# Performance work log

Measured on AMD Instinct MI355X. Metric: run time of the kernel, lower is better.

Reference implementation:

```python
import jax, jax.numpy as jnp
import numpy as np

N = 50000   # nodes
E = 800000  # edges
G = 256     # graphs in batch
NF, EF, H, L = 16, 8, 128, 4
EPS = 1e-5


def setup_inputs() -> dict:
    key = jax.random.key(0)
    ks = jax.random.split(key, 20)
    s = 0.05
    return {
        "x": jax.random.normal(ks[0], (N, NF), jnp.float32),
        "edge_index": jax.random.randint(ks[1], (2, E), 0, N, dtype=jnp.int32),
        "edge_attr": jax.random.uniform(ks[2], (E, EF), jnp.float32),
        "batch": jnp.sort(jax.random.randint(ks[3], (N,), 0, G, dtype=jnp.int32)),
        "W_emb": jax.random.normal(ks[4], (NF, H), jnp.float32) * s,
        "b_emb": jnp.zeros((H,), jnp.float32),
        "Wf": jax.random.normal(ks[5], (L, 2 * H + EF, H), jnp.float32) * s,
        "bf": jnp.zeros((L, H), jnp.float32),
        "Ws": jax.random.normal(ks[6], (L, 2 * H + EF, H), jnp.float32) * s,
        "bs": jnp.zeros((L, H), jnp.float32),
        "gamma": jnp.ones((L, H), jnp.float32),
        "beta": jnp.zeros((L, H), jnp.float32),
        "W1": jax.random.normal(ks[7], (H, 64), jnp.float32) * s,
        "b1": jnp.zeros((64,), jnp.float32),
        "W2": jax.random.normal(ks[8], (64, 32), jnp.float32) * s,
        "b2": jnp.zeros((32,), jnp.float32),
        "W_out": jax.random.normal(ks[9], (32, 1), jnp.float32) * s,
        "b_out": jnp.zeros((1,), jnp.float32),
    }


def reference(x, edge_index, edge_attr, batch, W_emb, b_emb, Wf, bf, Ws, bs,
              gamma, beta, W1, b1, W2, b2, W_out, b_out):
    src, dst = edge_index[0], edge_index[1]  # message j->i: x_j=h[src], x_i=h[dst]
    h = jax.nn.relu(x @ W_emb + b_emb)       # [N, H]
    for l in range(L):
        # CGConv: z_ij = [x_i, x_j, e_ij]; gated message; sum-aggregate; +x residual
        z = jnp.concatenate([h[dst], h[src], edge_attr], axis=-1)  # [E, 2H+EF]
        m = jax.nn.sigmoid(z @ Wf[l] + bf[l]) * jax.nn.softplus(z @ Ws[l] + bs[l])
        agg = jax.ops.segment_sum(m, dst, num_segments=N)
        x_new = agg + h
        # BatchNorm1d (training-mode batch statistics, biased var)
        mu = x_new.mean(axis=0)
        var = x_new.var(axis=0)
        x_new = gamma[l] * (x_new - mu) * jax.lax.rsqrt(var + EPS) + beta[l]
        x_new = jax.nn.relu(x_new)
        h = h + x_new
    # global mean pool over graphs
    cnt = jax.ops.segment_sum(jnp.ones((N,), h.dtype), batch, num_segments=G)
    pooled = jax.ops.segment_sum(h, batch, num_segments=G) / jnp.maximum(cnt, 1.0)[:, None]
    g = jax.nn.relu(pooled @ W1 + b1)
    g = jax.nn.relu(g @ W2 + b2)
    return (g @ W_out + b_out).squeeze(-1)  # [G]
```

## Files before the change

kernel.cpp:

```cpp
#include <hip/hip_runtime.h>
#include <hip/hip_bf16.h>

#define H 128
#define EFD 8
#define NLAYER 4
#define ZDIM (2*H+EFD)

typedef float f32x2 __attribute__((ext_vector_type(2)));
typedef float f32x4 __attribute__((ext_vector_type(4)));
typedef short s16x8 __attribute__((ext_vector_type(8)));
typedef _Float16 f16x4 __attribute__((ext_vector_type(4)));

#define PKFMA_LO(acc, a, b) asm("v_pk_fma_f32 %0, %1, %2, %0 op_sel:[0,0,0] op_sel_hi:[0,1,1]" : "+v"(acc) : "v"(a), "v"(b))
#define PKFMA_HI(acc, a, b) asm("v_pk_fma_f32 %0, %1, %2, %0 op_sel:[1,0,0] op_sel_hi:[1,1,1]" : "+v"(acc) : "v"(a), "v"(b))
#define PKFMA_LO_INIT(dst, a, b, c) asm("v_pk_fma_f32 %0, %1, %2, %3 op_sel:[0,0,0] op_sel_hi:[0,1,1]" : "=v"(dst) : "v"(a), "v"(b), "v"(c))

#define L2E 1.44269504088896340736f
#define LN2 0.69314718055994530942f

__device__ __forceinline__ unsigned short f2bf(float x){
    unsigned u = __float_as_uint(x);
    return (unsigned short)((u + 0x7FFFu + ((u>>16)&1u)) >> 16);
}

__global__ void embed_kernel(const float* __restrict__ x, const float* __restrict__ We,
                             const float* __restrict__ be, float* __restrict__ h, int N){
    int idx = blockIdx.x*blockDim.x + threadIdx.x;
    if (idx >= N*H) return;
    int n = idx >> 7, f = idx & 127;
    float a = be[f];
    #pragma unroll
    for (int k=0;k<16;k++) a = fmaf(x[n*16+k], We[k*H+f], a);
    h[idx] = fmaxf(a, 0.f);
}

__global__ void hist_kernel(const int* __restrict__ dstI, int* __restrict__ counts, int E){
    int e = blockIdx.x*blockDim.x + threadIdx.x;
    if (e < E) atomicAdd(&counts[dstI[e]], 1);
}

__global__ __launch_bounds__(1024) void scan1(const int* __restrict__ counts, int* __restrict__ incl,
                                              int* __restrict__ bsums, int N){
    __shared__ int lds[1024];
    int t = threadIdx.x;
    int i = blockIdx.x*1024 + t;
    int v = (i < N) ? counts[i] : 0;
    lds[t] = v;
    __syncthreads();
    for (int off=1; off<1024; off<<=1){
        int add = (t>=off) ? lds[t-off] : 0;
        __syncthreads();
        lds[t] += add;
        __syncthreads();
    }
    if (i < N) incl[i] = lds[t];
    if (t == 1023) bsums[blockIdx.x] = lds[1023];
}

__global__ void scan2(int* bsums, int nb){
    if (threadIdx.x == 0){
        int run = 0;
        for (int b=0;b<nb;b++){ int v = bsums[b]; bsums[b] = run; run += v; }
    }
}

__global__ __launch_bounds__(1024) void scan3(const int* incl, const int* __restrict__ counts,
                                              const int* __restrict__ bsums, int* __restrict__ rowptr,
                                              int* cursor, int N, int E){
    int i = blockIdx.x*1024 + threadIdx.x;
    if (i >= N) return;
    int ex = incl[i] - counts[i] + bsums[blockIdx.x];
    rowptr[i] = ex;
    cursor[i] = ex;
    if (i == N-1) rowptr[N] = E;
}

__global__ void scatter_kernel(const int* __restrict__ srcI, const int* __restrict__ dstI,
                               const float* __restrict__ eattr, int* __restrict__ cursor,
                               int* __restrict__ src_s, float* __restrict__ ea_s, int E){
    int e = blockIdx.x*blockDim.x + threadIdx.x;
    if (e >= E) return;
    int d = dstI[e];
    int pos = atomicAdd(&cursor[d], 1);
    src_s[pos] = srcI[e];
    const float4* s4 = (const float4*)(eattr + (size_t)e*EFD);
    float4* o4 = (float4*)(ea_s + (size_t)pos*EFD);
    o4[0] = s4[0]; o4[1] = s4[1];
}

__global__ __launch_bounds__(256) void wpack_kernel(const float* __restrict__ Wf, const float* __restrict__ Ws,
        s16x8* __restrict__ bhi, s16x8* __restrict__ blo){
    int idx = blockIdx.x*256 + threadIdx.x;
    int l = idx & 63, ct = (idx>>6)&7, ks = (idx>>9)&3, w = (idx>>11)&3, layer = idx>>13;
    int cp = w*128 + ct*16 + (l&15);
    int k0 = ks*32 + ((l>>4)<<3);
    const float* WfL = Wf + (size_t)layer*ZDIM*H;
    const float* WsL = Ws + (size_t)layer*ZDIM*H;
    int colIn = cp & 127;
    int sel = cp >> 7;
    const float* Wm = (sel & 1) ? WsL : WfL;
    int krow = (sel >> 1) ? H : 0;
    s16x8 vh, vl;
    #pragma unroll
    for (int e=0;e<8;e++){
        float v = Wm[(size_t)(krow + k0 + e)*H + colIn];
        unsigned short hb = f2bf(v);
        float rem = v - __uint_as_float(((unsigned)hb)<<16);
        vh[e] = (short)hb;
        vl[e] = (short)f2bf(rem);
    }
    bhi[idx] = vh;
    blo[idx] = vl;
}

__global__ __launch_bounds__(512, 2) void table_mfma(
        float* __restrict__ h, const float* __restrict__ xn, const float* __restrict__ scsh,
        const s16x8* __restrict__ bhi, const s16x8* __restrict__ blo,
        const float* __restrict__ bf_l, const float* __restrict__ bs_l,
        float* __restrict__ TD, _Float16* __restrict__ TS16, int N, int layer, int ntiles){
    __shared__ __align__(16) short amat[2][32*136];
    const int t = threadIdx.x;
    const int lane = t & 63, W = t >> 6;
    const int ow = W >> 1, ctbase = (W & 1)*4;
    const int rbase = lane & 15, kg = lane >> 4;

    s16x8 Bh[4][4], Bl[4][4];
    {
        const size_t bbase = ((size_t)layer*4 + ow)*2048;
        #pragma unroll
        for (int ks=0;ks<4;ks++)
            #pragma unroll
            for (int c=0;c<4;c++){
                Bh[ks][c] = bhi[bbase + ks*512 + (ctbase+c)*64 + lane];
                Bl[ks][c] = blo[bbase + ks*512 + (ctbase+c)*64 + lane];
            }
        #pragma unroll
        for (int ks=0;ks<4;ks++)
            #pragma unroll
            for (int c=0;c<4;c++) asm volatile("" : "+v"(Bh[ks][c]), "+v"(Bl[ks][c]));
    }
    int c_local[4], off16[4];
    float bv[4];
    #pragma unroll
    for (int c=0;c<4;c++){
        c_local[c] = (ctbase+c)*16 + rbase;
        off16[c] = (c_local[c] >> 1)*4 + ((ow & 1) << 1) + (c_local[c] & 1);
        bv[c] = (ow == 0) ? bf_l[c_local[c]]*L2E : (ow == 1) ? bs_l[c_local[c]]*L2E : 0.f;
    }
    const int srow = t >> 4;
    const int kb = (t & 15)*8;
    float sc8[8], sh8[8];
    if (scsh){
        #pragma unroll
        for (int q=0;q<8;q+=4){
            *(float4*)&sc8[q] = *(const float4*)(scsh + kb + q);
            *(float4*)&sh8[q] = *(const float4*)(scsh + H + kb + q);
        }
    }

    for (int tile = blockIdx.x; tile < ntiles; tile += gridDim.x){
        const int n0 = tile*32;
        {
            const int gn = n0 + srow;
            const bool valid = gn < N;
            float* hr = h + (size_t)gn*H + kb;
            float vv[8];
            if (scsh){
                const float* xr = xn + (size_t)gn*H + kb;
                #pragma unroll
                for (int q=0;q<8;q+=4){
                    float4 xv = valid ? *(const float4*)(xr + q) : make_float4(0.f,0.f,0.f,0.f);
                    float4 hv = valid ? *(const float4*)(hr + q) : make_float4(0.f,0.f,0.f,0.f);
                    vv[q]   = hv.x + fmaxf(fmaf(xv.x, sc8[q],   sh8[q]),   0.f);
                    vv[q+1] = hv.y + fmaxf(fmaf(xv.y, sc8[q+1], sh8[q+1]), 0.f);
                    vv[q+2] = hv.z + fmaxf(fmaf(xv.z, sc8[q+2], sh8[q+2]), 0.f);
                    vv[q+3] = hv.w + fmaxf(fmaf(xv.w, sc8[q+3], sh8[q+3]), 0.f);
                }
                if (valid){
                    #pragma unroll
                    for (int q=0;q<8;q+=4){
                        float4 o; o.x=vv[q]; o.y=vv[q+1]; o.z=vv[q+2]; o.w=vv[q+3];
                        *(float4*)(hr + q) = o;
                    }
                }
            } else {
                #pragma unroll
                for (int q=0;q<8;q+=4){
                    float4 hv = valid ? *(const float4*)(hr + q) : make_float4(0.f,0.f,0.f,0.f);
                    vv[q]=hv.x; vv[q+1]=hv.y; vv[q+2]=hv.z; vv[q+3]=hv.w;
                }
            }
            s16x8 hv2, lv2;
            #pragma unroll
            for (int q=0;q<8;q++){
                unsigned short hb = f2bf(vv[q]);
                float rem = vv[q] - __uint_as_float(((unsigned)hb)<<16);
                hv2[q] = (short)hb;
                lv2[q] = (short)f2bf(rem);
            }
            *(s16x8*)&amat[0][srow*136 + kb] = hv2;
            *(s16x8*)&amat[1][srow*136 + kb] = lv2;
        }
        __syncthreads();
        f32x4 acc[2][4];
        #pragma unroll
        for (int rt=0;rt<2;rt++)
            #pragma unroll
            for (int c=0;c<4;c++){ acc[rt][c][0]=0.f; acc[rt][c][1]=0.f; acc[rt][c][2]=0.f; acc[rt][c][3]=0.f; }
        #pragma unroll
        for (int ks=0;ks<4;ks++){
            s16x8 ah[2], al[2];
            #pragma unroll
            for (int rt=0;rt<2;rt++){
                const int ao = (rbase + 16*rt)*136 + ks*32 + kg*8;
                ah[rt] = *(const s16x8*)&amat[0][ao];
                al[rt] = *(const s16x8*)&amat[1][ao];
            }
            #pragma unroll
            for (int c=0;c<4;c++)
                #pragma unroll
                for (int rt=0;rt<2;rt++){
                    acc[rt][c] = __builtin_amdgcn_mfma_f32_16x16x32_bf16(ah[rt], Bh[ks][c], acc[rt][c], 0, 0, 0);
                    acc[rt][c] = __builtin_amdgcn_mfma_f32_16x16x32_bf16(ah[rt], Bl[ks][c], acc[rt][c], 0, 0, 0);
                    acc[rt][c] = __builtin_amdgcn_mfma_f32_16x16x32_bf16(al[rt], Bh[ks][c], acc[rt][c], 0, 0, 0);
                }
        }
        if (ow < 2){
            const int colbase = (ow & 1)*128;
            #pragma unroll
            for (int c=0;c<4;c++)
                #pragma unroll
                for (int rt=0;rt<2;rt++){
                    const int nrow0 = n0 + 16*rt + kg*4;
                    #pragma unroll
                    for (int r=0;r<4;r++){
                        const int nd = nrow0 + r;
                        if (nd < N) TD[(size_t)nd*256 + colbase + c_local[c]] = fmaf(acc[rt][c][r], L2E, bv[c]);
                    }
                }
        } else {
            #pragma unroll
            for (int c=0;c<4;c++)
                #pragma unroll
                for (int rt=0;rt<2;rt++){
                    const int nrow0 = n0 + 16*rt + kg*4;
                    #pragma unroll
                    for (int r=0;r<4;r++){
                        const int nd = nrow0 + r;
                        if (nd < N) TS16[(size_t)nd*256 + off16[c]] = (_Float16)(acc[rt][c][r]*L2E);
                    }
                }
        }
        __syncthreads();
    }
}

__global__ __launch_bounds__(256, 4) void agg_kernel(
        const float* __restrict__ TD, const _Float16* __restrict__ TS16,
        const int* __restrict__ rowptr, const int* __restrict__ src_s, const float* __restrict__ ea_s,
        const float* __restrict__ Wf_l, const float* __restrict__ Ws_l,
        const float* __restrict__ h, float* __restrict__ xn, int N){
    __shared__ float wE[2048];
    const int t = threadIdx.x;
    {
        const float4* a = (const float4*)(Wf_l + 2*H*H);
        const float4* b = (const float4*)(Ws_l + 2*H*H);
        float4 va = a[t], vb = b[t];
        va.x*=L2E; va.y*=L2E; va.z*=L2E; va.w*=L2E;
        vb.x*=L2E; vb.y*=L2E; vb.z*=L2E; vb.w*=L2E;
        ((float4*)wE)[t] = va;
        ((float4*)wE)[256 + t] = vb;
    }
    __syncthreads();
    const int k = t & 63;
    const int i = blockIdx.x*4 + (t >> 6);
    if (i >= N) return;
    f32x2 wef2[8], wes2[8];
    #pragma unroll
    for (int r=0;r<8;r++){
        wef2[r] = *(const f32x2*)&wE[r*128 + 2*k];
        wes2[r] = *(const f32x2*)&wE[1024 + r*128 + 2*k];
    }
    #pragma unroll
    for (int r=0;r<8;r++) asm volatile("" : "+v"(wef2[r]), "+v"(wes2[r]));
    const f32x2* td = (const f32x2*)(TD + ((size_t)i << 8));
    f32x2 fd2 = td[k], sd2 = td[64+k];
    f32x2 acc = {0.f, 0.f};
    const int e0 = __builtin_amdgcn_readfirstlane(rowptr[i]);
    const int e1 = __builtin_amdgcn_readfirstlane(rowptr[i+1]);
    const int myoff = 4*k;
    int j = (e0 < e1) ? __builtin_amdgcn_readfirstlane(src_s[e0]) : 0;
    f16x4 tv = *(const f16x4*)(TS16 + (((size_t)(unsigned)j) << 8) + myoff);
    for (int e = e0; e < e1; ++e){
        const int en = (e+1 < e1) ? (e+1) : e;
        const int jn = __builtin_amdgcn_readfirstlane(src_s[en]);
        f16x4 tvn = *(const f16x4*)(TS16 + (((size_t)(unsigned)jn) << 8) + myoff);
        const float* ep = ea_s + (size_t)e*EFD;
        f32x4 eaA = *(const f32x4*)(ep);
        f32x4 eaB = *(const f32x4*)(ep + 4);
        f32x2 ea0 = __builtin_shufflevector(eaA, eaA, 0, 1);
        f32x2 ea1 = __builtin_shufflevector(eaA, eaA, 2, 3);
        f32x2 ea2 = __builtin_shufflevector(eaB, eaB, 0, 1);
        f32x2 ea3 = __builtin_shufflevector(eaB, eaB, 2, 3);
        f32x2 ef, es;
        PKFMA_LO_INIT(ef, ea0, wef2[0], fd2);
        PKFMA_HI(ef, ea0, wef2[1]);
        PKFMA_LO(ef, ea1, wef2[2]); PKFMA_HI(ef, ea1, wef2[3]);
        PKFMA_LO(ef, ea2, wef2[4]); PKFMA_HI(ef, ea2, wef2[5]);
        PKFMA_LO(ef, ea3, wef2[6]); PKFMA_HI(ef, ea3, wef2[7]);
        PKFMA_LO_INIT(es, ea0, wes2[0], sd2);
        PKFMA_HI(es, ea0, wes2[1]);
        PKFMA_LO(es, ea1, wes2[2]); PKFMA_HI(es, ea1, wes2[3]);
        PKFMA_LO(es, ea2, wes2[4]); PKFMA_HI(es, ea2, wes2[5]);
        PKFMA_LO(es, ea3, wes2[6]); PKFMA_HI(es, ea3, wes2[7]);
        f32x2 g = ef, p = es;
        g.x += (float)tv[0]; g.y += (float)tv[1];
        p.x += (float)tv[2]; p.y += (float)tv[3];
        float sx = __builtin_amdgcn_rcpf(1.0f + __builtin_amdgcn_exp2f(-g.x));
        float sy = __builtin_amdgcn_rcpf(1.0f + __builtin_amdgcn_exp2f(-g.y));
        float tx = fmaxf(p.x, 0.f) + __builtin_amdgcn_logf(1.0f + __builtin_amdgcn_exp2f(-fabsf(p.x)));
        float ty = fmaxf(p.y, 0.f) + __builtin_amdgcn_logf(1.0f + __builtin_amdgcn_exp2f(-fabsf(p.y)));
        acc.x = fmaf(sx*tx, LN2, acc.x);
        acc.y = fmaf(sy*ty, LN2, acc.y);
        tv = tvn; j = jn;
    }
    f32x2 hv = *(const f32x2*)(h + ((size_t)i << 7) + 2*k);
    f32x2 o = acc + hv;
    *(f32x2*)(xn + ((size_t)i << 7) + 2*k) = o;
}

__global__ __launch_bounds__(256) void stats_kernel(const float* __restrict__ xn, double* __restrict__ sums, int N){
    __shared__ double l1[128], l2[128];
    const int f = threadIdx.x & 127;
    const int half = threadIdx.x >> 7;
    const int nb = gridDim.x;
    const int per = (N + nb - 1)/nb;
    const int r0 = blockIdx.x*per;
    const int r1 = min(N, r0+per);
    double s = 0.0, s2 = 0.0;
    for (int r=r0+half; r<r1; r+=2){
        float v = xn[(size_t)r*H + f];
        s += v; s2 += (double)v*(double)v;
    }
    if (half == 1){ l1[f] = s; l2[f] = s2; }
    __syncthreads();
    if (half == 0){
        s += l1[f]; s2 += l2[f];
        atomicAdd(&sums[f], s);
        atomicAdd(&sums[H+f], s2);
    }
}

__global__ void finalize_bn(double* __restrict__ sums, const float* __restrict__ gamma_l,
                            const float* __restrict__ beta_l, float* __restrict__ scsh, int N){
    int f = threadIdx.x;
    if (f >= H) return;
    double mu = sums[f]/(double)N;
    double var = sums[H+f]/(double)N - mu*mu;
    if (var < 0.0) var = 0.0;
    float sc = (float)((double)gamma_l[f] / sqrt(var + 1e-5));
    scsh[f]   = sc;
    scsh[H+f] = (float)((double)beta_l[f] - mu*(double)sc);
    sums[f] = 0.0;
    sums[H+f] = 0.0;
}

__global__ __launch_bounds__(128) void pool_mlp_kernel(const float* __restrict__ h, const float* __restrict__ xn,
        const float* __restrict__ scsh, const int* __restrict__ batch,
        const float* __restrict__ W1, const float* __restrict__ b1,
        const float* __restrict__ W2, const float* __restrict__ b2,
        const float* __restrict__ Wo, const float* __restrict__ bo,
        float* __restrict__ out, int N){
    __shared__ float row[128];
    __shared__ float g1[64];
    __shared__ float g2[32];
    const int g = blockIdx.x;
    const int t = threadIdx.x;
    int lo = 0, hi = N;
    while (lo < hi){ int m = (lo+hi)>>1; if (batch[m] < g) lo = m+1; else hi = m; }
    const int s0 = lo;
    hi = N;
    while (lo < hi){ int m = (lo+hi)>>1; if (batch[m] < g+1) lo = m+1; else hi = m; }
    const int s1 = lo;
    const float sc = scsh[t], sh = scsh[H+t];
    float acc = 0.f;
    for (int r = s0; r < s1; ++r){
        float hv = h[(size_t)r*H + t];
        float xv = xn[(size_t)r*H + t];
        acc += hv + fmaxf(fmaf(xv, sc, sh), 0.f);
    }
    const float inv = 1.0f/fmaxf((float)(s1-s0), 1.0f);
    row[t] = acc*inv;
    __syncthreads();
    if (t < 64){
        float a = b1[t];
        #pragma unroll 4
        for (int i2=0;i2<128;i2++) a = fmaf(row[i2], W1[i2*64+t], a);
        g1[t] = fmaxf(a, 0.f);
    }
    __syncthreads();
    if (t < 32){
        float b = b2[t];
        #pragma unroll 4
        for (int i2=0;i2<64;i2++) b = fmaf(g1[i2], W2[i2*32+t], b);
        g2[t] = fmaxf(b, 0.f);
    }
    __syncthreads();
    if (t < 64){
        float p = (t < 32) ? g2[t]*Wo[t] : 0.f;
        for (int off=32; off>0; off>>=1) p += __shfl_down(p, off);
        if (t == 0) out[g] = p + bo[0];
    }
}

extern "C" void kernel_launch(void* const* d_in, const int* in_sizes, int n_in,
                              void* d_out, int out_size, void* d_ws, size_t ws_size,
                              hipStream_t stream){
    const float* x     = (const float*)d_in[0];
    const int*   eidx  = (const int*)d_in[1];
    const float* eattr = (const float*)d_in[2];
    const int*   batch = (const int*)d_in[3];
    const float* W_emb = (const float*)d_in[4];
    const float* b_emb = (const float*)d_in[5];
    const float* Wf    = (const float*)d_in[6];
    const float* bf    = (const float*)d_in[7];
    const float* Wsm   = (const float*)d_in[8];
    const float* bs    = (const float*)d_in[9];
    const float* gamma = (const float*)d_in[10];
    const float* beta  = (const float*)d_in[11];
    const float* W1    = (const float*)d_in[12];
    const float* b1    = (const float*)d_in[13];
    const float* W2    = (const float*)d_in[14];
    const float* b2    = (const float*)d_in[15];
    const float* Wo    = (const float*)d_in[16];
    const float* bo    = (const float*)d_in[17];
    float* out = (float*)d_out;

    const int N = in_sizes[0]/16;
    const int E = in_sizes[1]/2;
    const int G = out_size;

    const int* srcI = eidx;
    const int* dstI = eidx + E;

    char* p = (char*)d_ws;
    auto alloc = [&](size_t bytes)->char*{ char* r = p; p += (bytes + 255) & ~255ull; return r; };
    float*     h      = (float*)     alloc((size_t)N*H*4);
    float*     xn     = (float*)     alloc((size_t)N*H*4);
    float*     TD     = (float*)     alloc((size_t)N*2*H*4);
    _Float16*  TS16   = (_Float16*)  alloc((size_t)N*2*H*2);
    float*     ea_s   = (float*)     alloc((size_t)E*EFD*4);
    int*       src_s  = (int*)       alloc((size_t)E*4);
    int*       rowptr = (int*)       alloc((size_t)(N+1)*4);
    int*       cursor = (int*)       alloc((size_t)N*4);
    int*       counts = (int*)       alloc((size_t)N*4);
    int*       bsums  = (int*)       alloc(256*4);
    double*    sums   = (double*)    alloc(2*H*8);
    float*     scsh   = (float*)     alloc(2*H*4);
    s16x8*     bhi    = (s16x8*)     alloc((size_t)NLAYER*8192*16);
    s16x8*     blo    = (s16x8*)     alloc((size_t)NLAYER*8192*16);

    const int thr = 256;
    hipMemsetAsync(counts, 0, (size_t)N*4, stream);
    hipMemsetAsync(sums, 0, 2*H*8, stream);
    embed_kernel<<<(N*H + thr-1)/thr, thr, 0, stream>>>(x, W_emb, b_emb, h, N);
    hist_kernel<<<(E + thr-1)/thr, thr, 0, stream>>>(dstI, counts, E);
    int nb = (N + 1023)/1024;
    scan1<<<nb, 1024, 0, stream>>>(counts, cursor, bsums, N);
    scan2<<<1, 64, 0, stream>>>(bsums, nb);
    scan3<<<nb, 1024, 0, stream>>>(cursor, counts, bsums, rowptr, cursor, N, E);
    scatter_kernel<<<(E + thr-1)/thr, thr, 0, stream>>>(srcI, dstI, eattr, cursor, src_s, ea_s, E);
    wpack_kernel<<<128, 256, 0, stream>>>(Wf, Wsm, bhi, blo);

    const int ntiles = (N + 31)/32;
    for (int l=0;l<NLAYER;l++){
        const float* Wf_l = Wf  + (size_t)l*ZDIM*H;
        const float* Ws_l = Wsm + (size_t)l*ZDIM*H;
        table_mfma<<<256, 512, 0, stream>>>(h, xn, (l==0)?nullptr:scsh, bhi, blo,
                                            bf + l*H, bs + l*H, TD, TS16, N, l, ntiles);
        agg_kernel<<<(N+3)/4, 256, 0, stream>>>(TD, TS16, rowptr, src_s, ea_s, Wf_l, Ws_l, h, xn, N);
        stats_kernel<<<256, 256, 0, stream>>>(xn, sums, N);
        finalize_bn<<<1, 128, 0, stream>>>(sums, gamma + l*H, beta + l*H, scsh, N);
    }

    pool_mlp_kernel<<<G, 128, 0, stream>>>(h, xn, scsh, batch, W1, b1, W2, b2, Wo, bo, out, N);
}
```

Before: 866.6 us.

## Merge dst/src tables into single fp16 row-interleaved table with deeper prefetch

Replaces the fp32 dst-side table and the separate fp16 src-side table with one fp16 table of 512 halfs per node, dst part first and src part second. The per-node gather in agg then reads a single row region and moves half the bytes for the dst part. The agg loop prefetches two edges ahead and drops the readfirstlane on src indices. table_mfma software-prefetches the next tile's h/xn rows, launches 512 blocks instead of 256, and agg occupancy goes from 4 to 6. Storing the dst-side logits in fp16 reduces their precision, which may affect accuracy.

Measured after the change: 918.5 us. +6.0%, slower.

```diff
diff --git a/kernel.cpp b/kernel.cpp
--- a/kernel.cpp
+++ b/kernel.cpp
@@ -117,7 +117,7 @@
         float* __restrict__ h, const float* __restrict__ xn, const float* __restrict__ scsh,
         const s16x8* __restrict__ bhi, const s16x8* __restrict__ blo,
         const float* __restrict__ bf_l, const float* __restrict__ bs_l,
-        float* __restrict__ TD, _Float16* __restrict__ TS16, int N, int layer, int ntiles){
+        _Float16* __restrict__ T16, int N, int layer, int ntiles){
     __shared__ __align__(16) short amat[2][32*136];
     const int t = threadIdx.x;
     const int lane = t & 63, W = t >> 6;
@@ -139,13 +139,13 @@
             #pragma unroll
             for (int c=0;c<4;c++) asm volatile("" : "+v"(Bh[ks][c]), "+v"(Bl[ks][c]));
     }
-    int c_local[4], off16[4];
+    int offT[4];
     float bv[4];
     #pragma unroll
     for (int c=0;c<4;c++){
-        c_local[c] = (ctbase+c)*16 + rbase;
-        off16[c] = (c_local[c] >> 1)*4 + ((ow & 1) << 1) + (c_local[c] & 1);
-        bv[c] = (ow == 0) ? bf_l[c_local[c]]*L2E : (ow == 1) ? bs_l[c_local[c]]*L2E : 0.f;
+        const int cl = (ctbase+c)*16 + rbase;
+        offT[c] = (ow>>1)*256 + ((cl>>1)<<2) + ((ow&1)<<1) + (cl&1);
+        bv[c] = (ow == 0) ? bf_l[cl]*L2E : (ow == 1) ? bs_l[cl]*L2E : 0.f;
     }
     const int srow = t >> 4;
     const int kb = (t & 15)*8;
@@ -158,37 +158,44 @@
         }
     }
 
-    for (int tile = blockIdx.x; tile < ntiles; tile += gridDim.x){
+    const int stride = gridDim.x;
+    int tile = blockIdx.x;
+    float4 ph0, ph1, px0, px1;
+    auto PREF = [&](int tl){
+        const int gn = tl*32 + srow;
+        const bool v = (gn < N);
+        const float* hr = h + (size_t)gn*H + kb;
+        ph0 = v ? *(const float4*)(hr)     : make_float4(0.f,0.f,0.f,0.f);
+        ph1 = v ? *(const float4*)(hr + 4) : make_float4(0.f,0.f,0.f,0.f);
+        if (scsh){
+            const float* xr = xn + (size_t)gn*H + kb;
+            px0 = v ? *(const float4*)(xr)     : make_float4(0.f,0.f,0.f,0.f);
+            px1 = v ? *(const float4*)(xr + 4) : make_float4(0.f,0.f,0.f,0.f);
+        }
+    };
+    PREF(tile);
+    for (; tile < ntiles; tile += stride){
         const int n0 = tile*32;
         {
             const int gn = n0 + srow;
             const bool valid = gn < N;
-            float* hr = h + (size_t)gn*H + kb;
             float vv[8];
             if (scsh){
-                const float* xr = xn + (size_t)gn*H + kb;
                 #pragma unroll
-                for (int q=0;q<8;q+=4){
-                    float4 xv = valid ? *(const float4*)(xr + q) : make_float4(0.f,0.f,0.f,0.f);
-                    float4 hv = valid ? *(const float4*)(hr + q) : make_float4(0.f,0.f,0.f,0.f);
-                    vv[q]   = hv.x + fmaxf(fmaf(xv.x, sc8[q],   sh8[q]),   0.f);
-                    vv[q+1] = hv.y + fmaxf(fmaf(xv.y, sc8[q+1], sh8[q+1]), 0.f);
-                    vv[q+2] = hv.z + fmaxf(fmaf(xv.z, sc8[q+2], sh8[q+2]), 0.f);
-                    vv[q+3] = hv.w + fmaxf(fmaf(xv.w, sc8[q+3], sh8[q+3]), 0.f);
+                for (int q=0;q<4;q++){
+                    vv[q]   = (&ph0.x)[q] + fmaxf(fmaf((&px0.x)[q], sc8[q],   sh8[q]),   0.f);
+                    vv[q+4] = (&ph1.x)[q] + fmaxf(fmaf((&px1.x)[q], sc8[q+4], sh8[q+4]), 0.f);
                 }
                 if (valid){
-                    #pragma unroll
-                    for (int q=0;q<8;q+=4){
-                        float4 o; o.x=vv[q]; o.y=vv[q+1]; o.z=vv[q+2]; o.w=vv[q+3];
-                        *(float4*)(hr + q) = o;
-                    }
+                    float* hr = h + (size_t)gn*H + kb;
+                    float4 o0; o0.x=vv[0]; o0.y=vv[1]; o0.z=vv[2]; o0.w=vv[3];
+                    float4 o1; o1.x=vv[4]; o1.y=vv[5]; o1.z=vv[6]; o1.w=vv[7];
+                    *(float4*)(hr)     = o0;
+                    *(float4*)(hr + 4) = o1;
                 }
             } else {
                 #pragma unroll
-                for (int q=0;q<8;q+=4){
-                    float4 hv = valid ? *(const float4*)(hr + q) : make_float4(0.f,0.f,0.f,0.f);
-                    vv[q]=hv.x; vv[q+1]=hv.y; vv[q+2]=hv.z; vv[q+3]=hv.w;
-                }
+                for (int q=0;q<4;q++){ vv[q] = (&ph0.x)[q]; vv[q+4] = (&ph1.x)[q]; }
             }
             s16x8 hv2, lv2;
             #pragma unroll
@@ -202,6 +209,7 @@
             *(s16x8*)&amat[1][srow*136 + kb] = lv2;
         }
         __syncthreads();
+        PREF(tile + stride);
         f32x4 acc[2][4];
         #pragma unroll
         for (int rt=0;rt<2;rt++)
@@ -225,38 +233,23 @@
                     acc[rt][c] = __builtin_amdgcn_mfma_f32_16x16x32_bf16(al[rt], Bh[ks][c], acc[rt][c], 0, 0, 0);
                 }
         }
-        if (ow < 2){
-            const int colbase = (ow & 1)*128;
-            #pragma unroll
-            for (int c=0;c<4;c++)
+        #pragma unroll
+        for (int c=0;c<4;c++)
+            #pragma unroll
+            for (int rt=0;rt<2;rt++){
+                const int nrow0 = n0 + 16*rt + kg*4;
                 #pragma unroll
-                for (int rt=0;rt<2;rt++){
-                    const int nrow0 = n0 + 16*rt + kg*4;
-                    #pragma unroll
-                    for (int r=0;r<4;r++){
-                        const int nd = nrow0 + r;
-                        if (nd < N) TD[(size_t)nd*256 + colbase + c_local[c]] = fmaf(acc[rt][c][r], L2E, bv[c]);
-                    }
+                for (int r=0;r<4;r++){
+                    const int nd = nrow0 + r;
+                    if (nd < N) T16[(size_t)nd*512 + offT[c]] = (_Float16)fmaf(acc[rt][c][r], L2E, bv[c]);
                 }
-        } else {
-            #pragma unroll
-            for (int c=0;c<4;c++)
-                #pragma unroll
-                for (int rt=0;rt<2;rt++){
-                    const int nrow0 = n0 + 16*rt + kg*4;
-                    #pragma unroll
-                    for (int r=0;r<4;r++){
-                        const int nd = nrow0 + r;
-                        if (nd < N) TS16[(size_t)nd*256 + off16[c]] = (_Float16)(acc[rt][c][r]*L2E);
-                    }
-                }
-        }
+            }
         __syncthreads();
     }
 }
 
-__global__ __launch_bounds__(256, 4) void agg_kernel(
-        const float* __restrict__ TD, const _Float16* __restrict__ TS16,
+__global__ __launch_bounds__(256, 6) void agg_kernel(
+        const _Float16* __restrict__ T16,
         const int* __restrict__ rowptr, const int* __restrict__ src_s, const float* __restrict__ ea_s,
         const float* __restrict__ Wf_l, const float* __restrict__ Ws_l,
         const float* __restrict__ h, float* __restrict__ xn, int N){
@@ -283,18 +276,22 @@
     }
     #pragma unroll
     for (int r=0;r<8;r++) asm volatile("" : "+v"(wef2[r]), "+v"(wes2[r]));
-    const f32x2* td = (const f32x2*)(TD + ((size_t)i << 8));
-    f32x2 fd2 = td[k], sd2 = td[64+k];
+    f16x4 dv = *(const f16x4*)(T16 + ((size_t)i << 9) + 4*k);
+    f32x2 fd2, sd2;
+    fd2.x = (float)dv[0]; fd2.y = (float)dv[1];
+    sd2.x = (float)dv[2]; sd2.y = (float)dv[3];
     f32x2 acc = {0.f, 0.f};
     const int e0 = __builtin_amdgcn_readfirstlane(rowptr[i]);
     const int e1 = __builtin_amdgcn_readfirstlane(rowptr[i+1]);
-    const int myoff = 4*k;
-    int j = (e0 < e1) ? __builtin_amdgcn_readfirstlane(src_s[e0]) : 0;
-    f16x4 tv = *(const f16x4*)(TS16 + (((size_t)(unsigned)j) << 8) + myoff);
+    const _Float16* Ts = T16 + 256 + 4*k;
+    const int j0 = (e0 < e1) ? src_s[e0] : 0;
+    const int j1 = (e0+1 < e1) ? src_s[e0+1] : j0;
+    f16x4 tvA = *(const f16x4*)(Ts + ((size_t)(unsigned)j0 << 9));
+    f16x4 tvB = *(const f16x4*)(Ts + ((size_t)(unsigned)j1 << 9));
     for (int e = e0; e < e1; ++e){
-        const int en = (e+1 < e1) ? (e+1) : e;
-        const int jn = __builtin_amdgcn_readfirstlane(src_s[en]);
-        f16x4 tvn = *(const f16x4*)(TS16 + (((size_t)(unsigned)jn) << 8) + myoff);
+        const int ec = (e+2 < e1) ? (e+2) : (e1-1);
+        const int jn = src_s[ec];
+        f16x4 tvC = *(const f16x4*)(Ts + ((size_t)(unsigned)jn << 9));
         const float* ep = ea_s + (size_t)e*EFD;
         f32x4 eaA = *(const f32x4*)(ep);
         f32x4 eaB = *(const f32x4*)(ep + 4);
@@ -314,15 +311,15 @@
         PKFMA_LO(es, ea2, wes2[4]); PKFMA_HI(es, ea2, wes2[5]);
         PKFMA_LO(es, ea3, wes2[6]); PKFMA_HI(es, ea3, wes2[7]);
         f32x2 g = ef, p = es;
-        g.x += (float)tv[0]; g.y += (float)tv[1];
-        p.x += (float)tv[2]; p.y += (float)tv[3];
+        g.x += (float)tvA[0]; g.y += (float)tvA[1];
+        p.x += (float)tvA[2]; p.y += (float)tvA[3];
         float sx = __builtin_amdgcn_rcpf(1.0f + __builtin_amdgcn_exp2f(-g.x));
         float sy = __builtin_amdgcn_rcpf(1.0f + __builtin_amdgcn_exp2f(-g.y));
         float tx = fmaxf(p.x, 0.f) + __builtin_amdgcn_logf(1.0f + __builtin_amdgcn_exp2f(-fabsf(p.x)));
         float ty = fmaxf(p.y, 0.f) + __builtin_amdgcn_logf(1.0f + __builtin_amdgcn_exp2f(-fabsf(p.y)));
         acc.x = fmaf(sx*tx, LN2, acc.x);
         acc.y = fmaf(sy*ty, LN2, acc.y);
-        tv = tvn; j = jn;
+        tvA = tvB; tvB = tvC;
     }
     f32x2 hv = *(const f32x2*)(h + ((size_t)i << 7) + 2*k);
     f32x2 o = acc + hv;
@@ -447,8 +444,7 @@
     auto alloc = [&](size_t bytes)->char*{ char* r = p; p += (bytes + 255) & ~255ull; return r; };
     float*     h      = (float*)     alloc((size_t)N*H*4);
     float*     xn     = (float*)     alloc((size_t)N*H*4);
-    float*     TD     = (float*)     alloc((size_t)N*2*H*4);
-    _Float16*  TS16   = (_Float16*)  alloc((size_t)N*2*H*2);
+    _Float16*  T16    = (_Float16*)  alloc((size_t)N*512*2);
     float*     ea_s   = (float*)     alloc((size_t)E*EFD*4);
     int*       src_s  = (int*)       alloc((size_t)E*4);
     int*       rowptr = (int*)       alloc((size_t)(N+1)*4);
@@ -476,9 +472,9 @@
     for (int l=0;l<NLAYER;l++){
         const float* Wf_l = Wf  + (size_t)l*ZDIM*H;
         const float* Ws_l = Wsm + (size_t)l*ZDIM*H;
-        table_mfma<<<256, 512, 0, stream>>>(h, xn, (l==0)?nullptr:scsh, bhi, blo,
-                                            bf + l*H, bs + l*H, TD, TS16, N, l, ntiles);
-        agg_kernel<<<(N+3)/4, 256, 0, stream>>>(TD, TS16, rowptr, src_s, ea_s, Wf_l, Ws_l, h, xn, N);
+        table_mfma<<<512, 512, 0, stream>>>(h, xn, (l==0)?nullptr:scsh, bhi, blo,
+                                            bf + l*H, bs + l*H, T16, N, l, ntiles);
+        agg_kernel<<<(N+3)/4, 256, 0, stream>>>(T16, rowptr, src_s, ea_s, Wf_l, Ws_l, h, xn, N);
         stats_kernel<<<256, 256, 0, stream>>>(xn, sums, N);
         finalize_bn<<<1, 128, 0, stream>>>(sums, gamma + l*H, beta + l*H, scsh, N);
     }
```
